# Performance work log

Measured on AMD Instinct MI355X. Metric: run time of the kernel, lower is better.

## Reference

```python
import jax, jax.numpy as jnp
import numpy as np

N = 25000      # nodes
E = 200000     # edges (avg degree 8)
DIN = 512      # input_dim
HID = 512      # hidden_dim


def setup_inputs() -> dict:
    key = jax.random.key(0)
    ks = jax.random.split(key, 8)
    x = jax.random.normal(ks[0], (N, DIN), jnp.float32)
    edge_index = jax.random.randint(ks[1], (2, E), 0, N, jnp.int32)
    s_in = 1.0 / np.sqrt(DIN).astype(np.float32)
    s_h = 1.0 / np.sqrt(HID).astype(np.float32)
    W1 = jax.random.normal(ks[2], (DIN, HID), jnp.float32) * s_in
    b1 = jnp.zeros((HID,), jnp.float32)
    W2 = jax.random.normal(ks[3], (HID, HID), jnp.float32) * s_h
    b2 = jnp.zeros((HID,), jnp.float32)
    Wo = jax.random.normal(ks[4], (HID, 1), jnp.float32) * s_h
    bo = jnp.zeros((1,), jnp.float32)
    Ww = jax.random.normal(ks[5], (HID, 1), jnp.float32) * s_h
    bw = jnp.zeros((1,), jnp.float32)
    return dict(x=x, edge_index=edge_index, W1=W1, b1=b1, W2=W2, b2=b2,
                Wo=Wo, bo=bo, Ww=Ww, bw=bw)


def reference(x, edge_index, W1, b1, W2, b2, Wo, bo, Ww, bw):
    n = x.shape[0]
    src, dst = edge_index[0], edge_index[1]
    # GCNConv with self-loops: deg counts incoming edges + 1 self-loop
    deg = jax.ops.segment_sum(jnp.ones(src.shape[0], x.dtype), dst,
                              num_segments=n) + 1.0
    dis = jax.lax.rsqrt(deg)              # deg^{-1/2}, [N]
    norm = dis[src] * dis[dst]            # per-edge symmetric norm, [E]

    def gcn(h, W, b):
        hw = h @ W                        # [N, H] dense GEMM
        msg = hw[src] * norm[:, None]     # gather + scale, [E, H]
        agg = jax.ops.segment_sum(msg, dst, num_segments=n)
        agg = agg + hw * (dis * dis)[:, None]  # self-loop contribution
        return agg + b

    h1 = jax.nn.relu(gcn(x, W1, b1))
    h2 = jax.nn.relu(gcn(h1, W2, b2))
    open_logits = (h2 @ Wo + bo)[:, 0]
    wall_logits = (h2 @ Ww + bw)[:, 0]
    return open_logits, wall_logits
```

## Files before the change

### kernel.cpp

```cpp
#include <hip/hip_runtime.h>
#include <hip/hip_bf16.h>

#define DIN 512
#define HID 512

#define AS1 __attribute__((address_space(1)))
#define AS3 __attribute__((address_space(3)))

typedef __attribute__((ext_vector_type(8))) short bfrag;
typedef __attribute__((ext_vector_type(4))) float ffrag;
typedef __attribute__((ext_vector_type(8))) unsigned short u16x8;
typedef __attribute__((ext_vector_type(4))) unsigned short u16x4;

__global__ void count_kernel(const int* __restrict__ dst, int* __restrict__ cnt, int E) {
    int e = blockIdx.x * 256 + threadIdx.x;
    if (e >= E) return;
    atomicAdd(&cnt[dst[e]], 1);
}

__global__ __launch_bounds__(256) void scan1(const int* __restrict__ cnt, int* __restrict__ tmp,
                                             int* __restrict__ bsum, int N) {
    int tid = threadIdx.x, lane = tid & 63, wave = tid >> 6;
    int i = blockIdx.x * 256 + tid;
    int v = (i < N) ? cnt[i] : 0;
    int incl = v;
#pragma unroll
    for (int o = 1; o < 64; o <<= 1) {
        int t = __shfl_up(incl, o);
        if (lane >= o) incl += t;
    }
    __shared__ int wtot[4];
    if (lane == 63) wtot[wave] = incl;
    __syncthreads();
    int woff = 0;
#pragma unroll
    for (int w = 0; w < 4; ++w) woff += (w < wave) ? wtot[w] : 0;
    if (i < N) tmp[i] = woff + incl - v;
    if (tid == 255) bsum[blockIdx.x] = woff + incl;
}

__global__ void scan2(int* __restrict__ bsum, int nb) {
    int tid = threadIdx.x;
    int lane = tid & 63, wave = tid >> 6;
    int v = (tid < nb) ? bsum[tid] : 0;
    int incl = v;
#pragma unroll
    for (int o = 1; o < 64; o <<= 1) {
        int t = __shfl_up(incl, o);
        if (lane >= o) incl += t;
    }
    __shared__ int w0;
    if (tid == 63) w0 = incl;
    __syncthreads();
    int off = wave ? w0 : 0;
    if (tid < nb) bsum[tid] = off + incl - v;
    if (tid == 127) bsum[nb] = off + incl;
}

__global__ void scan3(const int* __restrict__ cnt, const int* __restrict__ tmp,
                      const int* __restrict__ bsum, int* __restrict__ offs,
                      float* __restrict__ dis, int N, int nb) {
    int i = blockIdx.x * 256 + threadIdx.x;
    if (i < N) {
        offs[i] = tmp[i] + bsum[i >> 8];
        dis[i] = rsqrtf((float)cnt[i] + 1.0f);
    }
    if (i == 0) offs[N] = bsum[nb];
}

__global__ void fill_kernel(const int* __restrict__ src, const int* __restrict__ dst,
                            const int* __restrict__ offs, int* __restrict__ cursor,
                            const float* __restrict__ dis,
                            int* __restrict__ csr, float* __restrict__ sdis, int E) {
    int e = blockIdx.x * 256 + threadIdx.x;
    if (e >= E) return;
    int d = dst[e];
    int s = src[e];
    int pos = offs[d] + atomicAdd(&cursor[d], 1);
    csr[pos] = s;
    sdis[pos] = dis[s];
}

__global__ __launch_bounds__(256) void convert_pad(const float* __restrict__ x,
                                                   unsigned short* __restrict__ xb,
                                                   int Nvalid) {
    int idx = blockIdx.x * 256 + threadIdx.x;
    int row = idx >> 6;
    int c = (idx & 63) * 8;
    unsigned short o[8];
    if (row < Nvalid) {
        float4 a = *(const float4*)&x[(size_t)row * 512 + c];
        float4 b = *(const float4*)&x[(size_t)row * 512 + c + 4];
        __hip_bfloat16 t;
        t = __float2bfloat16(a.x); o[0] = *(unsigned short*)&t;
        t = __float2bfloat16(a.y); o[1] = *(unsigned short*)&t;
        t = __float2bfloat16(a.z); o[2] = *(unsigned short*)&t;
        t = __float2bfloat16(a.w); o[3] = *(unsigned short*)&t;
        t = __float2bfloat16(b.x); o[4] = *(unsigned short*)&t;
        t = __float2bfloat16(b.y); o[5] = *(unsigned short*)&t;
        t = __float2bfloat16(b.z); o[6] = *(unsigned short*)&t;
        t = __float2bfloat16(b.w); o[7] = *(unsigned short*)&t;
    } else {
#pragma unroll
        for (int j = 0; j < 8; ++j) o[j] = 0;
    }
    *(u16x8*)&xb[(size_t)row * 512 + c] = *(u16x8*)o;
}

__global__ void transpose_cvt(const float* __restrict__ W, unsigned short* __restrict__ Wt) {
    __shared__ float t[32][33];
    int tx = threadIdx.x, ty = threadIdx.y;
    int n0 = blockIdx.x * 32, k0 = blockIdx.y * 32;
#pragma unroll
    for (int s = 0; s < 4; ++s)
        t[ty + 8 * s][tx] = W[(size_t)(k0 + ty + 8 * s) * 512 + n0 + tx];
    __syncthreads();
#pragma unroll
    for (int s = 0; s < 4; ++s) {
        __hip_bfloat16 b = __float2bfloat16(t[tx][ty + 8 * s]);
        Wt[(size_t)(n0 + ty + 8 * s) * 512 + k0 + tx] = *(unsigned short*)&b;
    }
}

__global__ __launch_bounds__(256) void gemm_bf16(const short* __restrict__ A,
                                                 const short* __restrict__ B,
                                                 unsigned short* __restrict__ C) {
    __shared__ __align__(16) short As[128 * 64];
    __shared__ __align__(16) short Bs[128 * 64];
    const int K = 512;
    int tid = threadIdx.x;
    int lane = tid & 63, wave = tid >> 6;
    int m0 = blockIdx.x * 128;
    int n0 = blockIdx.y * 128;
    int wm = (wave & 1) * 64;
    int wn = (wave >> 1) * 64;
    int r = lane & 15, q = lane >> 4;

    size_t aglob[4], bglob[4];
    int ldsoff[4];
#pragma unroll
    for (int i = 0; i < 4; ++i) {
        int s = i * 256 + tid;
        int row = s >> 3;
        int c = (s & 7) ^ (row & 7);
        aglob[i] = (size_t)(m0 + row) * K + c * 8;
        bglob[i] = (size_t)(n0 + row) * K + c * 8;
        ldsoff[i] = (i * 256 + (tid & ~63)) * 8;
    }

    ffrag acc[4][4];
#pragma unroll
    for (int i = 0; i < 4; ++i)
#pragma unroll
        for (int j = 0; j < 4; ++j) acc[i][j] = ffrag{0.f, 0.f, 0.f, 0.f};

    for (int k0 = 0; k0 < K; k0 += 64) {
#pragma unroll
        for (int i = 0; i < 4; ++i) {
            __builtin_amdgcn_global_load_lds((const AS1 void*)(A + aglob[i] + k0),
                                             (AS3 void*)(As + ldsoff[i]), 16, 0, 0);
            __builtin_amdgcn_global_load_lds((const AS1 void*)(B + bglob[i] + k0),
                                             (AS3 void*)(Bs + ldsoff[i]), 16, 0, 0);
        }
        __syncthreads();

#pragma unroll
        for (int s2 = 0; s2 < 2; ++s2) {
            bfrag af[4], bfr[4];
#pragma unroll
            for (int i = 0; i < 4; ++i) {
                int arow = wm + i * 16 + r;
                int ach = (s2 * 4 + q) ^ (arow & 7);
                af[i] = *(const bfrag*)&As[arow * 64 + ach * 8];
                int brow = wn + i * 16 + r;
                int bch = (s2 * 4 + q) ^ (brow & 7);
                bfr[i] = *(const bfrag*)&Bs[brow * 64 + bch * 8];
            }
#pragma unroll
            for (int i = 0; i < 4; ++i)
#pragma unroll
                for (int j = 0; j < 4; ++j)
                    acc[i][j] = __builtin_amdgcn_mfma_f32_16x16x32_bf16(bfr[j], af[i], acc[i][j], 0, 0, 0);
        }
        __syncthreads();
    }

#pragma unroll
    for (int i = 0; i < 4; ++i) {
        int m = m0 + wm + i * 16 + r;
#pragma unroll
        for (int j = 0; j < 4; ++j) {
            int n = n0 + wn + j * 16 + q * 4;
            u16x4 o;
#pragma unroll
            for (int reg = 0; reg < 4; ++reg) {
                __hip_bfloat16 b = __float2bfloat16(acc[i][j][reg]);
                o[reg] = *(unsigned short*)&b;
            }
            *(u16x4*)&C[(size_t)m * 512 + n] = o;
        }
    }
}

__device__ inline void cvt8(u16x8 v, float* f) {
#pragma unroll
    for (int j = 0; j < 8; ++j) f[j] = __uint_as_float((unsigned)v[j] << 16);
}

__global__ __launch_bounds__(256) void agg_relu(const unsigned short* __restrict__ hw,
                                                const int* __restrict__ csr,
                                                const float* __restrict__ sdis,
                                                const int* __restrict__ offs,
                                                const float* __restrict__ dis,
                                                const float* __restrict__ bias,
                                                unsigned short* __restrict__ out, int N) {
    int node = blockIdx.x * 4 + (threadIdx.x >> 6);
    if (node >= N) return;
    int lane = threadIdx.x & 63;
    int c0 = lane * 8;

    float dn = dis[node];
    int e0 = offs[node], e1 = offs[node + 1];

    float acc[8];
    {
        u16x8 sv = *(const u16x8*)&hw[(size_t)node * HID + c0];
        float g[8];
        cvt8(sv, g);
        float4 bb0 = *(const float4*)&bias[c0];
        float4 bb1 = *(const float4*)&bias[c0 + 4];
        float dis2 = dn * dn;
        acc[0] = g[0] * dis2 + bb0.x; acc[1] = g[1] * dis2 + bb0.y;
        acc[2] = g[2] * dis2 + bb0.z; acc[3] = g[3] * dis2 + bb0.w;
        acc[4] = g[4] * dis2 + bb1.x; acc[5] = g[5] * dis2 + bb1.y;
        acc[6] = g[6] * dis2 + bb1.z; acc[7] = g[7] * dis2 + bb1.w;
    }

    int e = e0;
    for (; e + 4 <= e1; e += 4) {
        int s0 = csr[e], s1 = csr[e + 1], s2 = csr[e + 2], s3 = csr[e + 3];
        float w0 = sdis[e] * dn, w1 = sdis[e + 1] * dn;
        float w2 = sdis[e + 2] * dn, w3 = sdis[e + 3] * dn;
        u16x8 v0 = *(const u16x8*)&hw[(size_t)s0 * HID + c0];
        u16x8 v1 = *(const u16x8*)&hw[(size_t)s1 * HID + c0];
        u16x8 v2 = *(const u16x8*)&hw[(size_t)s2 * HID + c0];
        u16x8 v3 = *(const u16x8*)&hw[(size_t)s3 * HID + c0];
        float g[8];
        cvt8(v0, g);
#pragma unroll
        for (int j = 0; j < 8; ++j) acc[j] += g[j] * w0;
        cvt8(v1, g);
#pragma unroll
        for (int j = 0; j < 8; ++j) acc[j] += g[j] * w1;
        cvt8(v2, g);
#pragma unroll
        for (int j = 0; j < 8; ++j) acc[j] += g[j] * w2;
        cvt8(v3, g);
#pragma unroll
        for (int j = 0; j < 8; ++j) acc[j] += g[j] * w3;
    }
    for (; e < e1; ++e) {
        int s = csr[e];
        float w = sdis[e] * dn;
        u16x8 v = *(const u16x8*)&hw[(size_t)s * HID + c0];
        float g[8];
        cvt8(v, g);
#pragma unroll
        for (int j = 0; j < 8; ++j) acc[j] += g[j] * w;
    }

    unsigned short o[8];
#pragma unroll
    for (int j = 0; j < 8; ++j) {
        __hip_bfloat16 b = __float2bfloat16(fmaxf(acc[j], 0.f));
        o[j] = *(unsigned short*)&b;
    }
    *(u16x8*)&out[(size_t)node * HID + c0] = *(u16x8*)o;
}

__global__ __launch_bounds__(256) void agg_relu_heads(const unsigned short* __restrict__ hw,
                                                      const int* __restrict__ csr,
                                                      const float* __restrict__ sdis,
                                                      const int* __restrict__ offs,
                                                      const float* __restrict__ dis,
                                                      const float* __restrict__ bias,
                                                      const float* __restrict__ Wo,
                                                      const float* __restrict__ bo,
                                                      const float* __restrict__ Ww,
                                                      const float* __restrict__ bw,
                                                      float* __restrict__ out, int N) {
    int node = blockIdx.x * 4 + (threadIdx.x >> 6);
    if (node >= N) return;
    int lane = threadIdx.x & 63;
    int c0 = lane * 8;

    float dn = dis[node];
    int e0 = offs[node], e1 = offs[node + 1];

    float acc[8];
    {
        u16x8 sv = *(const u16x8*)&hw[(size_t)node * HID + c0];
        float g[8];
        cvt8(sv, g);
        float4 bb0 = *(const float4*)&bias[c0];
        float4 bb1 = *(const float4*)&bias[c0 + 4];
        float dis2 = dn * dn;
        acc[0] = g[0] * dis2 + bb0.x; acc[1] = g[1] * dis2 + bb0.y;
        acc[2] = g[2] * dis2 + bb0.z; acc[3] = g[3] * dis2 + bb0.w;
        acc[4] = g[4] * dis2 + bb1.x; acc[5] = g[5] * dis2 + bb1.y;
        acc[6] = g[6] * dis2 + bb1.z; acc[7] = g[7] * dis2 + bb1.w;
    }

    int e = e0;
    for (; e + 4 <= e1; e += 4) {
        int s0 = csr[e], s1 = csr[e + 1], s2 = csr[e + 2], s3 = csr[e + 3];
        float w0 = sdis[e] * dn, w1 = sdis[e + 1] * dn;
        float w2 = sdis[e + 2] * dn, w3 = sdis[e + 3] * dn;
        u16x8 v0 = *(const u16x8*)&hw[(size_t)s0 * HID + c0];
        u16x8 v1 = *(const u16x8*)&hw[(size_t)s1 * HID + c0];
        u16x8 v2 = *(const u16x8*)&hw[(size_t)s2 * HID + c0];
        u16x8 v3 = *(const u16x8*)&hw[(size_t)s3 * HID + c0];
        float g[8];
        cvt8(v0, g);
#pragma unroll
        for (int j = 0; j < 8; ++j) acc[j] += g[j] * w0;
        cvt8(v1, g);
#pragma unroll
        for (int j = 0; j < 8; ++j) acc[j] += g[j] * w1;
        cvt8(v2, g);
#pragma unroll
        for (int j = 0; j < 8; ++j) acc[j] += g[j] * w2;
        cvt8(v3, g);
#pragma unroll
        for (int j = 0; j < 8; ++j) acc[j] += g[j] * w3;
    }
    for (; e < e1; ++e) {
        int s = csr[e];
        float w = sdis[e] * dn;
        u16x8 v = *(const u16x8*)&hw[(size_t)s * HID + c0];
        float g[8];
        cvt8(v, g);
#pragma unroll
        for (int j = 0; j < 8; ++j) acc[j] += g[j] * w;
    }

    float4 wo0 = *(const float4*)&Wo[c0];
    float4 wo1 = *(const float4*)&Wo[c0 + 4];
    float4 ww0 = *(const float4*)&Ww[c0];
    float4 ww1 = *(const float4*)&Ww[c0 + 4];
    float po = 0.f, pw = 0.f, h;
    h = fmaxf(acc[0], 0.f); po += h * wo0.x; pw += h * ww0.x;
    h = fmaxf(acc[1], 0.f); po += h * wo0.y; pw += h * ww0.y;
    h = fmaxf(acc[2], 0.f); po += h * wo0.z; pw += h * ww0.z;
    h = fmaxf(acc[3], 0.f); po += h * wo0.w; pw += h * ww0.w;
    h = fmaxf(acc[4], 0.f); po += h * wo1.x; pw += h * ww1.x;
    h = fmaxf(acc[5], 0.f); po += h * wo1.y; pw += h * ww1.y;
    h = fmaxf(acc[6], 0.f); po += h * wo1.z; pw += h * ww1.z;
    h = fmaxf(acc[7], 0.f); po += h * wo1.w; pw += h * ww1.w;

#pragma unroll
    for (int off = 32; off > 0; off >>= 1) {
        po += __shfl_down(po, off);
        pw += __shfl_down(pw, off);
    }
    if (lane == 0) {
        out[node]     = po + bo[0];
        out[N + node] = pw + bw[0];
    }
}

extern "C" void kernel_launch(void* const* d_in, const int* in_sizes, int n_in,
                              void* d_out, int out_size, void* d_ws, size_t ws_size,
                              hipStream_t stream) {
    const float* x  = (const float*)d_in[0];
    const int*   ei = (const int*)d_in[1];
    const float* W1 = (const float*)d_in[2];
    const float* b1 = (const float*)d_in[3];
    const float* W2 = (const float*)d_in[4];
    const float* b2 = (const float*)d_in[5];
    const float* Wo = (const float*)d_in[6];
    const float* bo = (const float*)d_in[7];
    const float* Ww = (const float*)d_in[8];
    const float* bw = (const float*)d_in[9];

    const int N = in_sizes[0] / DIN;
    const int E = in_sizes[1] / 2;
    const int Mpad = (N + 127) & ~127;
    const int nb = (N + 255) / 256;

    char* ws = (char*)d_ws;
    size_t p = 0;
    auto alloc = [&](size_t bytes) -> char* {
        char* r = ws + p;
        p += (bytes + 255) & ~(size_t)255;
        return r;
    };
    int*   cnt    = (int*)alloc((size_t)N * 4);
    int*   offs   = (int*)alloc((size_t)(N + 1) * 4);
    int*   cursor = (int*)alloc((size_t)N * 4);
    int*   tmp    = (int*)alloc((size_t)N * 4);
    int*   bsum   = (int*)alloc(132 * 4);
    float* dis    = (float*)alloc((size_t)N * 4);
    int*   csr    = (int*)alloc((size_t)E * 4);
    float* sdis   = (float*)alloc((size_t)E * 4);
    unsigned short* xb  = (unsigned short*)alloc((size_t)Mpad * 512 * 2);
    unsigned short* Wt1 = (unsigned short*)alloc((size_t)512 * 512 * 2);
    unsigned short* Wt2 = (unsigned short*)alloc((size_t)512 * 512 * 2);
    unsigned short* hw  = (unsigned short*)alloc((size_t)Mpad * 512 * 2);
    unsigned short* h1  = (unsigned short*)alloc((size_t)Mpad * 512 * 2);

    const int* src = ei;
    const int* dst = ei + E;

    hipMemsetAsync(cnt, 0, (size_t)N * 4, stream);
    hipMemsetAsync(cursor, 0, (size_t)N * 4, stream);
    if (Mpad > N)
        hipMemsetAsync(h1 + (size_t)N * 512, 0, (size_t)(Mpad - N) * 512 * 2, stream);

    count_kernel<<<(E + 255) / 256, 256, 0, stream>>>(dst, cnt, E);
    scan1<<<nb, 256, 0, stream>>>(cnt, tmp, bsum, N);
    scan2<<<1, 128, 0, stream>>>(bsum, nb);
    scan3<<<nb, 256, 0, stream>>>(cnt, tmp, bsum, offs, dis, N, nb);
    fill_kernel<<<(E + 255) / 256, 256, 0, stream>>>(src, dst, offs, cursor, dis, csr, sdis, E);

    convert_pad<<<(Mpad * 64) / 256, 256, 0, stream>>>(x, xb, N);
    transpose_cvt<<<dim3(16, 16), dim3(32, 8), 0, stream>>>(W1, Wt1);
    transpose_cvt<<<dim3(16, 16), dim3(32, 8), 0, stream>>>(W2, Wt2);

    dim3 ggrid(Mpad / 128, 4);
    gemm_bf16<<<ggrid, 256, 0, stream>>>((const short*)xb, (const short*)Wt1, hw);
    agg_relu<<<(N + 3) / 4, 256, 0, stream>>>(hw, csr, sdis, offs, dis, b1, h1, N);
    gemm_bf16<<<ggrid, 256, 0, stream>>>((const short*)h1, (const short*)Wt2, hw);
    agg_relu_heads<<<(N + 3) / 4, 256, 0, stream>>>(hw, csr, sdis, offs, dis, b2,
                                                    Wo, bo, Ww, bw, (float*)d_out, N);
}
```

Measured before the change: 263.0 us.

## Fuse x conversion into first GEMM, merge prelude kernels, widen gather unroll

The first GEMM now loads fp32 x straight into LDS and converts it to bf16 while building MFMA fragments, which removes the separate convert_pad pass and the xb buffer. The weight transposes and the degree count are merged into one prelude launch, and scan3 writes the cursor start offsets so the cursor memset and the offs lookup in fill go away. Padding rows of h1 are zeroed inside agg_relu instead of by a memset. The aggregation loops now gather 8 neighbours per iteration with clamped indices to keep more loads in flight. In exchange, the GEMM's A tile takes twice the LDS and does conversion work in the inner loop, and the 8-wide loop adds wasted loads on the tail.

```diff
diff --git a/kernel.cpp b/kernel.cpp
--- a/kernel.cpp
+++ b/kernel.cpp
@@ -12,10 +12,35 @@
 typedef __attribute__((ext_vector_type(8))) unsigned short u16x8;
 typedef __attribute__((ext_vector_type(4))) unsigned short u16x4;
 
-__global__ void count_kernel(const int* __restrict__ dst, int* __restrict__ cnt, int E) {
-    int e = blockIdx.x * 256 + threadIdx.x;
-    if (e >= E) return;
-    atomicAdd(&cnt[dst[e]], 1);
+__global__ __launch_bounds__(256) void prelude(const float* __restrict__ W1,
+                                               const float* __restrict__ W2,
+                                               unsigned short* __restrict__ Wt1,
+                                               unsigned short* __restrict__ Wt2,
+                                               const int* __restrict__ dst,
+                                               int* __restrict__ cnt, int E) {
+    int b = blockIdx.x;
+    if (b < 512) {
+        int which = b >> 8;
+        int bb = b & 255;
+        const float* W = which ? W2 : W1;
+        unsigned short* Wt = which ? Wt2 : Wt1;
+        __shared__ float t[32][33];
+        int tid = threadIdx.x;
+        int tx = tid & 31, ty = tid >> 5;
+        int n0 = (bb & 15) * 32, k0 = (bb >> 4) * 32;
+#pragma unroll
+        for (int s = 0; s < 4; ++s)
+            t[ty + 8 * s][tx] = W[(size_t)(k0 + ty + 8 * s) * 512 + n0 + tx];
+        __syncthreads();
+#pragma unroll
+        for (int s = 0; s < 4; ++s) {
+            __hip_bfloat16 v = __float2bfloat16(t[tx][ty + 8 * s]);
+            Wt[(size_t)(n0 + ty + 8 * s) * 512 + k0 + tx] = *(unsigned short*)&v;
+        }
+    } else {
+        int e = (b - 512) * 256 + threadIdx.x;
+        if (e < E) atomicAdd(&cnt[dst[e]], 1);
+    }
 }
 
 __global__ __launch_bounds__(256) void scan1(const int* __restrict__ cnt, int* __restrict__ tmp,
@@ -59,66 +84,134 @@
 
 __global__ void scan3(const int* __restrict__ cnt, const int* __restrict__ tmp,
                       const int* __restrict__ bsum, int* __restrict__ offs,
-                      float* __restrict__ dis, int N, int nb) {
+                      int* __restrict__ cursor, float* __restrict__ dis, int N, int nb) {
     int i = blockIdx.x * 256 + threadIdx.x;
     if (i < N) {
-        offs[i] = tmp[i] + bsum[i >> 8];
+        int o = tmp[i] + bsum[i >> 8];
+        offs[i] = o;
+        cursor[i] = o;
         dis[i] = rsqrtf((float)cnt[i] + 1.0f);
     }
     if (i == 0) offs[N] = bsum[nb];
 }
 
 __global__ void fill_kernel(const int* __restrict__ src, const int* __restrict__ dst,
-                            const int* __restrict__ offs, int* __restrict__ cursor,
-                            const float* __restrict__ dis,
+                            int* __restrict__ cursor, const float* __restrict__ dis,
                             int* __restrict__ csr, float* __restrict__ sdis, int E) {
     int e = blockIdx.x * 256 + threadIdx.x;
     if (e >= E) return;
     int d = dst[e];
     int s = src[e];
-    int pos = offs[d] + atomicAdd(&cursor[d], 1);
+    int pos = atomicAdd(&cursor[d], 1);
     csr[pos] = s;
     sdis[pos] = dis[s];
 }
 
-__global__ __launch_bounds__(256) void convert_pad(const float* __restrict__ x,
-                                                   unsigned short* __restrict__ xb,
-                                                   int Nvalid) {
-    int idx = blockIdx.x * 256 + threadIdx.x;
-    int row = idx >> 6;
-    int c = (idx & 63) * 8;
-    unsigned short o[8];
-    if (row < Nvalid) {
-        float4 a = *(const float4*)&x[(size_t)row * 512 + c];
-        float4 b = *(const float4*)&x[(size_t)row * 512 + c + 4];
-        __hip_bfloat16 t;
-        t = __float2bfloat16(a.x); o[0] = *(unsigned short*)&t;
-        t = __float2bfloat16(a.y); o[1] = *(unsigned short*)&t;
-        t = __float2bfloat16(a.z); o[2] = *(unsigned short*)&t;
-        t = __float2bfloat16(a.w); o[3] = *(unsigned short*)&t;
-        t = __float2bfloat16(b.x); o[4] = *(unsigned short*)&t;
-        t = __float2bfloat16(b.y); o[5] = *(unsigned short*)&t;
-        t = __float2bfloat16(b.z); o[6] = *(unsigned short*)&t;
-        t = __float2bfloat16(b.w); o[7] = *(unsigned short*)&t;
-    } else {
-#pragma unroll
-        for (int j = 0; j < 8; ++j) o[j] = 0;
-    }
-    *(u16x8*)&xb[(size_t)row * 512 + c] = *(u16x8*)o;
-}
-
-__global__ void transpose_cvt(const float* __restrict__ W, unsigned short* __restrict__ Wt) {
-    __shared__ float t[32][33];
-    int tx = threadIdx.x, ty = threadIdx.y;
-    int n0 = blockIdx.x * 32, k0 = blockIdx.y * 32;
-#pragma unroll
-    for (int s = 0; s < 4; ++s)
-        t[ty + 8 * s][tx] = W[(size_t)(k0 + ty + 8 * s) * 512 + n0 + tx];
-    __syncthreads();
-#pragma unroll
-    for (int s = 0; s < 4; ++s) {
-        __hip_bfloat16 b = __float2bfloat16(t[tx][ty + 8 * s]);
-        Wt[(size_t)(n0 + ty + 8 * s) * 512 + k0 + tx] = *(unsigned short*)&b;
+__device__ inline bfrag pack8(float4 a, float4 b) {
+    bfrag o;
+    __hip_bfloat16 t;
+    t = __float2bfloat16(a.x); o[0] = *(short*)&t;
+    t = __float2bfloat16(a.y); o[1] = *(short*)&t;
+    t = __float2bfloat16(a.z); o[2] = *(short*)&t;
+    t = __float2bfloat16(a.w); o[3] = *(short*)&t;
+    t = __float2bfloat16(b.x); o[4] = *(short*)&t;
+    t = __float2bfloat16(b.y); o[5] = *(short*)&t;
+    t = __float2bfloat16(b.z); o[6] = *(short*)&t;
+    t = __float2bfloat16(b.w); o[7] = *(short*)&t;
+    return o;
+}
+
+__global__ __launch_bounds__(256) void gemm_a32(const float* __restrict__ A,
+                                                const short* __restrict__ B,
+                                                unsigned short* __restrict__ C, int Nvalid) {
+    __shared__ __align__(16) float Asf[128 * 64];
+    __shared__ __align__(16) short Bs[128 * 64];
+    const int K = 512;
+    int tid = threadIdx.x;
+    int lane = tid & 63, wave = tid >> 6;
+    int m0 = blockIdx.x * 128;
+    int n0 = blockIdx.y * 128;
+    int wm = (wave & 1) * 64;
+    int wn = (wave >> 1) * 64;
+    int r = lane & 15, q = lane >> 4;
+
+    unsigned aoff[8]; int aldso[8];
+#pragma unroll
+    for (int i = 0; i < 8; ++i) {
+        int s = i * 256 + tid;
+        int row = s >> 4;
+        int c = (s & 15) ^ (row & 15);
+        int gr = m0 + row;
+        if (gr > Nvalid - 1) gr = Nvalid - 1;
+        aoff[i] = (unsigned)gr * K + c * 4;
+        aldso[i] = (i * 256 + (tid & ~63)) * 4;
+    }
+    unsigned boff[4]; int bldso[4];
+#pragma unroll
+    for (int i = 0; i < 4; ++i) {
+        int s = i * 256 + tid;
+        int row = s >> 3;
+        int c = (s & 7) ^ (row & 7);
+        boff[i] = (unsigned)(n0 + row) * K + c * 8;
+        bldso[i] = (i * 256 + (tid & ~63)) * 8;
+    }
+
+    ffrag acc[4][4];
+#pragma unroll
+    for (int i = 0; i < 4; ++i)
+#pragma unroll
+        for (int j = 0; j < 4; ++j) acc[i][j] = ffrag{0.f, 0.f, 0.f, 0.f};
+
+    for (int k0 = 0; k0 < K; k0 += 64) {
+#pragma unroll
+        for (int i = 0; i < 8; ++i)
+            __builtin_amdgcn_global_load_lds((const AS1 void*)(A + aoff[i] + k0),
+                                             (AS3 void*)(Asf + aldso[i]), 16, 0, 0);
+#pragma unroll
+        for (int i = 0; i < 4; ++i)
+            __builtin_amdgcn_global_load_lds((const AS1 void*)(B + boff[i] + k0),
+                                             (AS3 void*)(Bs + bldso[i]), 16, 0, 0);
+        __syncthreads();
+
+#pragma unroll
+        for (int s2 = 0; s2 < 2; ++s2) {
+            bfrag af[4], bfr[4];
+#pragma unroll
+            for (int i = 0; i < 4; ++i) {
+                int m = wm + i * 16 + r;
+                int c0 = s2 * 8 + q * 2;
+                int p0 = (c0 ^ (m & 15)) * 4;
+                int p1 = ((c0 + 1) ^ (m & 15)) * 4;
+                float4 f0 = *(const float4*)&Asf[m * 64 + p0];
+                float4 f1 = *(const float4*)&Asf[m * 64 + p1];
+                af[i] = pack8(f0, f1);
+                int brow = wn + i * 16 + r;
+                int bch = (s2 * 4 + q) ^ (brow & 7);
+                bfr[i] = *(const bfrag*)&Bs[brow * 64 + bch * 8];
+            }
+#pragma unroll
+            for (int i = 0; i < 4; ++i)
+#pragma unroll
+                for (int j = 0; j < 4; ++j)
+                    acc[i][j] = __builtin_amdgcn_mfma_f32_16x16x32_bf16(bfr[j], af[i], acc[i][j], 0, 0, 0);
+        }
+        __syncthreads();
+    }
+
+#pragma unroll
+    for (int i = 0; i < 4; ++i) {
+        int m = m0 + wm + i * 16 + r;
+#pragma unroll
+        for (int j = 0; j < 4; ++j) {
+            int n = n0 + wn + j * 16 + q * 4;
+            u16x4 o;
+#pragma unroll
+            for (int reg = 0; reg < 4; ++reg) {
+                __hip_bfloat16 v = __float2bfloat16(acc[i][j][reg]);
+                o[reg] = *(unsigned short*)&v;
+            }
+            *(u16x4*)&C[(size_t)m * 512 + n] = o;
+        }
     }
 }
 
@@ -136,16 +229,15 @@
     int wn = (wave >> 1) * 64;
     int r = lane & 15, q = lane >> 4;
 
-    size_t aglob[4], bglob[4];
-    int ldsoff[4];
+    unsigned aoff[4], boff[4]; int ldso[4];
 #pragma unroll
     for (int i = 0; i < 4; ++i) {
         int s = i * 256 + tid;
         int row = s >> 3;
         int c = (s & 7) ^ (row & 7);
-        aglob[i] = (size_t)(m0 + row) * K + c * 8;
-        bglob[i] = (size_t)(n0 + row) * K + c * 8;
-        ldsoff[i] = (i * 256 + (tid & ~63)) * 8;
+        aoff[i] = (unsigned)(m0 + row) * K + c * 8;
+        boff[i] = (unsigned)(n0 + row) * K + c * 8;
+        ldso[i] = (i * 256 + (tid & ~63)) * 8;
     }
 
     ffrag acc[4][4];
@@ -157,10 +249,10 @@
     for (int k0 = 0; k0 < K; k0 += 64) {
 #pragma unroll
         for (int i = 0; i < 4; ++i) {
-            __builtin_amdgcn_global_load_lds((const AS1 void*)(A + aglob[i] + k0),
-                                             (AS3 void*)(As + ldsoff[i]), 16, 0, 0);
-            __builtin_amdgcn_global_load_lds((const AS1 void*)(B + bglob[i] + k0),
-                                             (AS3 void*)(Bs + ldsoff[i]), 16, 0, 0);
+            __builtin_amdgcn_global_load_lds((const AS1 void*)(A + aoff[i] + k0),
+                                             (AS3 void*)(As + ldso[i]), 16, 0, 0);
+            __builtin_amdgcn_global_load_lds((const AS1 void*)(B + boff[i] + k0),
+                                             (AS3 void*)(Bs + ldso[i]), 16, 0, 0);
         }
         __syncthreads();
 
@@ -194,8 +286,8 @@
             u16x4 o;
 #pragma unroll
             for (int reg = 0; reg < 4; ++reg) {
-                __hip_bfloat16 b = __float2bfloat16(acc[i][j][reg]);
-                o[reg] = *(unsigned short*)&b;
+                __hip_bfloat16 v = __float2bfloat16(acc[i][j][reg]);
+                o[reg] = *(unsigned short*)&v;
             }
             *(u16x4*)&C[(size_t)m * 512 + n] = o;
         }
@@ -213,11 +305,18 @@
                                                 const int* __restrict__ offs,
                                                 const float* __restrict__ dis,
                                                 const float* __restrict__ bias,
-                                                unsigned short* __restrict__ out, int N) {
+                                                unsigned short* __restrict__ out,
+                                                int N, int Mpad) {
     int node = blockIdx.x * 4 + (threadIdx.x >> 6);
-    if (node >= N) return;
     int lane = threadIdx.x & 63;
     int c0 = lane * 8;
+    if (node >= N) {
+        if (node < Mpad) {
+            u16x8 z = {0, 0, 0, 0, 0, 0, 0, 0};
+            *(u16x8*)&out[(size_t)node * HID + c0] = z;
+        }
+        return;
+    }
 
     float dn = dis[node];
     int e0 = offs[node], e1 = offs[node + 1];
@@ -236,37 +335,26 @@
         acc[6] = g[6] * dis2 + bb1.z; acc[7] = g[7] * dis2 + bb1.w;
     }
 
-    int e = e0;
-    for (; e + 4 <= e1; e += 4) {
-        int s0 = csr[e], s1 = csr[e + 1], s2 = csr[e + 2], s3 = csr[e + 3];
-        float w0 = sdis[e] * dn, w1 = sdis[e + 1] * dn;
-        float w2 = sdis[e + 2] * dn, w3 = sdis[e + 3] * dn;
-        u16x8 v0 = *(const u16x8*)&hw[(size_t)s0 * HID + c0];
-        u16x8 v1 = *(const u16x8*)&hw[(size_t)s1 * HID + c0];
-        u16x8 v2 = *(const u16x8*)&hw[(size_t)s2 * HID + c0];
-        u16x8 v3 = *(const u16x8*)&hw[(size_t)s3 * HID + c0];
-        float g[8];
-        cvt8(v0, g);
-#pragma unroll
-        for (int j = 0; j < 8; ++j) acc[j] += g[j] * w0;
-        cvt8(v1, g);
-#pragma unroll
-        for (int j = 0; j < 8; ++j) acc[j] += g[j] * w1;
-        cvt8(v2, g);
-#pragma unroll
-        for (int j = 0; j < 8; ++j) acc[j] += g[j] * w2;
-        cvt8(v3, g);
-#pragma unroll
-        for (int j = 0; j < 8; ++j) acc[j] += g[j] * w3;
-    }
-    for (; e < e1; ++e) {
-        int s = csr[e];
-        float w = sdis[e] * dn;
-        u16x8 v = *(const u16x8*)&hw[(size_t)s * HID + c0];
-        float g[8];
-        cvt8(v, g);
-#pragma unroll
-        for (int j = 0; j < 8; ++j) acc[j] += g[j] * w;
+    for (int e = e0; e < e1; e += 8) {
+        int idx[8]; float wgt[8];
+#pragma unroll
+        for (int j = 0; j < 8; ++j) {
+            int ee = e + j;
+            int ec = (ee < e1) ? ee : (e1 - 1);
+            idx[j] = csr[ec];
+            wgt[j] = (ee < e1) ? sdis[ec] * dn : 0.f;
+        }
+        u16x8 v[8];
+#pragma unroll
+        for (int j = 0; j < 8; ++j)
+            v[j] = *(const u16x8*)&hw[(size_t)idx[j] * HID + c0];
+#pragma unroll
+        for (int j = 0; j < 8; ++j) {
+            float g[8];
+            cvt8(v[j], g);
+#pragma unroll
+            for (int t = 0; t < 8; ++t) acc[t] += g[t] * wgt[j];
+        }
     }
 
     unsigned short o[8];
@@ -311,37 +399,26 @@
         acc[6] = g[6] * dis2 + bb1.z; acc[7] = g[7] * dis2 + bb1.w;
     }
 
-    int e = e0;
-    for (; e + 4 <= e1; e += 4) {
-        int s0 = csr[e], s1 = csr[e + 1], s2 = csr[e + 2], s3 = csr[e + 3];
-        float w0 = sdis[e] * dn, w1 = sdis[e + 1] * dn;
-        float w2 = sdis[e + 2] * dn, w3 = sdis[e + 3] * dn;
-        u16x8 v0 = *(const u16x8*)&hw[(size_t)s0 * HID + c0];
-        u16x8 v1 = *(const u16x8*)&hw[(size_t)s1 * HID + c0];
-        u16x8 v2 = *(const u16x8*)&hw[(size_t)s2 * HID + c0];
-        u16x8 v3 = *(const u16x8*)&hw[(size_t)s3 * HID + c0];
-        float g[8];
-        cvt8(v0, g);
-#pragma unroll
-        for (int j = 0; j < 8; ++j) acc[j] += g[j] * w0;
-        cvt8(v1, g);
-#pragma unroll
-        for (int j = 0; j < 8; ++j) acc[j] += g[j] * w1;
-        cvt8(v2, g);
-#pragma unroll
-        for (int j = 0; j < 8; ++j) acc[j] += g[j] * w2;
-        cvt8(v3, g);
-#pragma unroll
-        for (int j = 0; j < 8; ++j) acc[j] += g[j] * w3;
-    }
-    for (; e < e1; ++e) {
-        int s = csr[e];
-        float w = sdis[e] * dn;
-        u16x8 v = *(const u16x8*)&hw[(size_t)s * HID + c0];
-        float g[8];
-        cvt8(v, g);
-#pragma unroll
-        for (int j = 0; j < 8; ++j) acc[j] += g[j] * w;
+    for (int e = e0; e < e1; e += 8) {
+        int idx[8]; float wgt[8];
+#pragma unroll
+        for (int j = 0; j < 8; ++j) {
+            int ee = e + j;
+            int ec = (ee < e1) ? ee : (e1 - 1);
+            idx[j] = csr[ec];
+            wgt[j] = (ee < e1) ? sdis[ec] * dn : 0.f;
+        }
+        u16x8 v[8];
+#pragma unroll
+        for (int j = 0; j < 8; ++j)
+            v[j] = *(const u16x8*)&hw[(size_t)idx[j] * HID + c0];
+#pragma unroll
+        for (int j = 0; j < 8; ++j) {
+            float g[8];
+            cvt8(v[j], g);
+#pragma unroll
+            for (int t = 0; t < 8; ++t) acc[t] += g[t] * wgt[j];
+        }
     }
 
     float4 wo0 = *(const float4*)&Wo[c0];
@@ -401,9 +478,8 @@
     int*   tmp    = (int*)alloc((size_t)N * 4);
     int*   bsum   = (int*)alloc(132 * 4);
     float* dis    = (float*)alloc((size_t)N * 4);
-    int*   csr    = (int*)alloc((size_t)E * 4);
-    float* sdis   = (float*)alloc((size_t)E * 4);
-    unsigned short* xb  = (unsigned short*)alloc((size_t)Mpad * 512 * 2);
+    int*   csr    = (int*)alloc((size_t)E * 4 + 64);
+    float* sdis   = (float*)alloc((size_t)E * 4 + 64);
     unsigned short* Wt1 = (unsigned short*)alloc((size_t)512 * 512 * 2);
     unsigned short* Wt2 = (unsigned short*)alloc((size_t)512 * 512 * 2);
     unsigned short* hw  = (unsigned short*)alloc((size_t)Mpad * 512 * 2);
@@ -413,23 +489,16 @@
     const int* dst = ei + E;
 
     hipMemsetAsync(cnt, 0, (size_t)N * 4, stream);
-    hipMemsetAsync(cursor, 0, (size_t)N * 4, stream);
-    if (Mpad > N)
-        hipMemsetAsync(h1 + (size_t)N * 512, 0, (size_t)(Mpad - N) * 512 * 2, stream);
-
-    count_kernel<<<(E + 255) / 256, 256, 0, stream>>>(dst, cnt, E);
+
+    prelude<<<512 + (E + 255) / 256, 256, 0, stream>>>(W1, W2, Wt1, Wt2, dst, cnt, E);
     scan1<<<nb, 256, 0, stream>>>(cnt, tmp, bsum, N);
     scan2<<<1, 128, 0, stream>>>(bsum, nb);
-    scan3<<<nb, 256, 0, stream>>>(cnt, tmp, bsum, offs, dis, N, nb);
-    fill_kernel<<<(E + 255) / 256, 256, 0, stream>>>(src, dst, offs, cursor, dis, csr, sdis, E);
-
-    convert_pad<<<(Mpad * 64) / 256, 256, 0, stream>>>(x, xb, N);
-    transpose_cvt<<<dim3(16, 16), dim3(32, 8), 0, stream>>>(W1, Wt1);
-    transpose_cvt<<<dim3(16, 16), dim3(32, 8), 0, stream>>>(W2, Wt2);
+    scan3<<<nb, 256, 0, stream>>>(cnt, tmp, bsum, offs, cursor, dis, N, nb);
+    fill_kernel<<<(E + 255) / 256, 256, 0, stream>>>(src, dst, cursor, dis, csr, sdis, E);
 
     dim3 ggrid(Mpad / 128, 4);
-    gemm_bf16<<<ggrid, 256, 0, stream>>>((const short*)xb, (const short*)Wt1, hw);
-    agg_relu<<<(N + 3) / 4, 256, 0, stream>>>(hw, csr, sdis, offs, dis, b1, h1, N);
+    gemm_a32<<<ggrid, 256, 0, stream>>>(x, (const short*)Wt1, hw, N);
+    agg_relu<<<(Mpad + 3) / 4, 256, 0, stream>>>(hw, csr, sdis, offs, dis, b1, h1, N, Mpad);
     gemm_bf16<<<ggrid, 256, 0, stream>>>((const short*)h1, (const short*)Wt2, hw);
     agg_relu_heads<<<(N + 3) / 4, 256, 0, stream>>>(hw, csr, sdis, offs, dis, b2,
                                                     Wo, bo, Ww, bw, (float*)d_out, N);
```

Result: no change. 264.7 us (+0.6%).
